# Kernel optimization log

Measured on AMD Instinct MI355X. Metric: run time of the kernel, lower is better.

The kernel has to match this reference:

```python
import jax, jax.numpy as jnp
import numpy as np

G, S, F, H, C, L = 32, 2048, 128, 128, 40, 3
N = G * S           # 65536 nodes
E = N * 16          # 1048576 edges


def setup_inputs() -> dict:
    key = jax.random.key(0)
    ks = jax.random.split(key, 10)
    x = jax.random.normal(ks[0], (N, F), dtype=jnp.float32)
    edge_index = jax.random.randint(ks[1], (2, E), 0, N, dtype=jnp.int64)
    E_meta = jax.random.normal(ks[2], (G, H), dtype=jnp.float32)
    ptr = (jnp.arange(G + 1, dtype=jnp.int64) * S)  # uniform partitions
    # learned params (xavier-ish scaling)
    w0 = jax.random.normal(ks[3], (F, 1), dtype=jnp.float32) * (2.0 / (F + 1)) ** 0.5
    b0 = jax.random.normal(ks[4], (F, H), dtype=jnp.float32) * (2.0 / (F + H)) ** 0.5
    conv_w = jax.random.normal(ks[5], (L, H, H), dtype=jnp.float32) * (1.0 / H) ** 0.5
    conv_b = jnp.zeros((L, H), dtype=jnp.float32)
    lt1_w = jax.random.normal(ks[6], (C, H), dtype=jnp.float32) * (1.0 / H) ** 0.5
    lt1_b = jnp.zeros((C,), dtype=jnp.float32)
    return {"x": x, "edge_index": edge_index, "E_meta": E_meta, "ptr": ptr,
            "w0": w0, "b0": b0, "conv_w": conv_w, "conv_b": conv_b,
            "lt1_w": lt1_w, "lt1_b": lt1_b}


def _gcn_conv(h, src, dst, deg_inv_sqrt, W, b):
    # GCNConv (PyG defaults): h' = D^-1/2 (A+I) D^-1/2 (h W) + b
    hw = h @ W                                          # [N,H]
    norm = deg_inv_sqrt[src] * deg_inv_sqrt[dst]        # [E+N]
    msg = hw[src] * norm[:, None]                       # gather + scale
    return jax.ops.segment_sum(msg, dst, num_segments=h.shape[0]) + b


def reference(x, edge_index, E_meta, ptr, w0, b0, conv_w, conv_b, lt1_w, lt1_b):
    n_nodes = x.shape[0]
    g = E_meta.shape[0]
    s = n_nodes // g  # uniform ptr (ptr[i] = i*s) by construction
    # per-partition dynamic weight: relu(w0 @ emb^T + b0) -> [G,F,H]
    Wdyn = jax.nn.relu(w0[None, :, :] * E_meta[:, None, :] + b0[None, :, :])
    # segment matmul x[ptr[i]:ptr[i+1]] @ Wdyn[i], concatenated -> [N,H]
    h = jnp.einsum('gsf,gfh->gsh', x.reshape(g, s, -1), Wdyn).reshape(n_nodes, -1)
    # add self loops once; symmetric normalization on target degree
    loop = jnp.arange(n_nodes, dtype=edge_index.dtype)
    src = jnp.concatenate([edge_index[0], loop])
    dst = jnp.concatenate([edge_index[1], loop])
    deg = jax.ops.segment_sum(jnp.ones_like(dst, dtype=h.dtype), dst,
                              num_segments=n_nodes)
    deg_inv_sqrt = jnp.where(deg > 0, jax.lax.rsqrt(deg), 0.0)
    for l in range(conv_w.shape[0]):
        h = jax.nn.relu(_gcn_conv(h, src, dst, deg_inv_sqrt, conv_w[l], conv_b[l]))
        # F.dropout with training=False is identity (eval mode)
    logits = h @ lt1_w.T + lt1_b
    return jax.nn.log_softmax(logits, axis=1)
```

## Files before the change

### kernel.cpp

```cpp
#include <hip/hip_runtime.h>

#define NNODES 65536
#define NEDGES 1048576
#define HDIM 128
#define NCLS 40
#define BCAP 6144

#define FP8_SCALE 32.0f
#define FP8_INV   0.03125f

typedef unsigned int uint;
typedef __attribute__((ext_vector_type(8))) short bf16x8;
typedef __attribute__((ext_vector_type(4))) float f32x4;
typedef __attribute__((ext_vector_type(2))) float f32x2;

__device__ __forceinline__ float bf_lo(uint v) {
    return __builtin_bit_cast(float, v << 16);
}
__device__ __forceinline__ float bf_hi(uint v) {
    return __builtin_bit_cast(float, v & 0xffff0000u);
}
__device__ __forceinline__ uint pack_bf16x2(float a, float b) {
    uint ua = __builtin_bit_cast(uint, a);
    uint ub = __builtin_bit_cast(uint, b);
    ua += 0x7fff + ((ua >> 16) & 1);
    ub += 0x7fff + ((ub >> 16) & 1);
    return (ua >> 16) | (ub & 0xffff0000u);
}
__device__ __forceinline__ float tobf(float v) {
    uint u = __builtin_bit_cast(uint, v);
    u += 0x7fff + ((u >> 16) & 1);
    return __builtin_bit_cast(float, u & 0xffff0000u);
}

__device__ __forceinline__ f32x2 fp8_pair(uint u) {
    return __builtin_amdgcn_cvt_pk_f32_fp8((int)u, false);
}

__global__ __launch_bounds__(256) void convT_kernel(
    const float* __restrict__ cw, uint* __restrict__ WT, int* __restrict__ gcursor,
    const float* __restrict__ ltw, uint* __restrict__ WcT8)
{
    int t = threadIdx.x;
    if (blockIdx.x == 0) gcursor[t] = 0;
    int idx = blockIdx.x * 256 + t;
    if (idx < 24576) {
        int ip = idx & 63;
        int o = (idx >> 6) & 127;
        int l = idx >> 13;
        int i0 = ip * 2;
        float v0 = cw[l * 16384 + i0 * 128 + o];
        float v1 = cw[l * 16384 + (i0 + 1) * 128 + o];
        WT[idx] = pack_bf16x2(v0, v1);
    } else {
        int idx2 = idx - 24576;
        int part = (idx2 >= 3072) ? 1 : 0;
        int r = idx2 - part * 3072;
        int o = r >> 6;
        int ip = r & 63;
        float v0 = 0.f, v1 = 0.f;
        if (o < NCLS) {
            float w0v = ltw[o * 128 + ip * 2];
            float w1v = ltw[o * 128 + ip * 2 + 1];
            float h0 = tobf(w0v), h1 = tobf(w1v);
            if (part == 0) { v0 = h0; v1 = h1; }
            else { v0 = w0v - h0; v1 = w1v - h1; }
        }
        WcT8[idx2] = pack_bf16x2(v0, v1);
    }
}

__global__ __launch_bounds__(256) void bucket_scatter(
    const int* __restrict__ src, const int* __restrict__ dst,
    int* __restrict__ gcursor, uint* __restrict__ binned)
{
    __shared__ int lcnt[256];
    __shared__ int lbase[256];
    int t = threadIdx.x;
    int base = blockIdx.x * 4096;
    lcnt[t] = 0;
    __syncthreads();
    uint e[16];
#pragma unroll
    for (int k = 0; k < 16; k++) {
        int i = base + k * 256 + t;
        uint s = (uint)src[i];
        uint d = (uint)dst[i];
        e[k] = (d << 16) | s;
        atomicAdd(&lcnt[d >> 8], 1);
    }
    __syncthreads();
    lbase[t] = t * BCAP + atomicAdd(&gcursor[t], lcnt[t]);
    lcnt[t] = 0;
    __syncthreads();
#pragma unroll
    for (int k = 0; k < 16; k++) {
        int b = e[k] >> 24;
        int r = atomicAdd(&lcnt[b], 1);
        binned[lbase[b] + r] = e[k];
    }
}

__global__ __launch_bounds__(256) void prep_kernel(
    const uint* __restrict__ binned, const int* __restrict__ gcursor,
    int* __restrict__ row_beg, int* __restrict__ row_end4,
    float* __restrict__ dis, int* __restrict__ csr,
    const float* __restrict__ w0, const float* __restrict__ em,
    const float* __restrict__ b0, const uint* __restrict__ convwT0,
    uint* __restrict__ WT)
{
    __shared__ int cnt[256];
    __shared__ int tmp[256];
    __shared__ int fb[256];
    const int t = threadIdx.x;

    if (blockIdx.x < 256) {
        int b = blockIdx.x;
        int e0 = b * BCAP, e1 = e0 + gcursor[b];
        cnt[t] = 0;
        __syncthreads();
        for (int i = e0 + t; i < e1; i += 256)
            atomicAdd(&cnt[(binned[i] >> 16) & 255], 1);
        __syncthreads();
        int v = cnt[t];
        int size4 = (v + 3) & ~3;
        tmp[t] = size4;
        __syncthreads();
        for (int off = 1; off < 256; off <<= 1) {
            int u = (t >= off) ? tmp[t - off] : 0;
            __syncthreads();
            tmp[t] += u;
            __syncthreads();
        }
        fb[t] = tmp[t] - size4;
        int node = (b << 8) + t;
        int beg = e0 + fb[t];
        row_beg[node] = beg;
        row_end4[node] = beg + size4;
        dis[node] = rsqrtf((float)(v + 1));
        for (int p = v; p < size4; p++) csr[beg + p] = NNODES;
        cnt[t] = 0;
        __syncthreads();
        for (int i = e0 + t; i < e1; i += 256) {
            uint e = binned[i];
            int d = (e >> 16) & 255;
            int r = atomicAdd(&cnt[d], 1);
            csr[e0 + fb[d] + r] = (int)(e & 0xffffu);
        }
    } else {
        int bb = blockIdx.x - 256;
        const int g = bb >> 3;
        const int c = bb & 7;
        const int wave = t >> 6;
        const int lane = t & 63;
        const int q = lane >> 4;
        const int l16 = lane & 15;
        const float* emg = em + g * 128;

        f32x4 acc[2];
#pragma unroll
        for (int r = 0; r < 2; r++) {
            acc[r][0] = 0.f; acc[r][1] = 0.f; acc[r][2] = 0.f; acc[r][3] = 0.f;
        }
        const int f = c * 16 + l16;
        const float wf = w0[f];

#pragma unroll
        for (int k0 = 0; k0 < 128; k0 += 32) {
            const int kf = k0 + q * 8;
            bf16x8 afrag[2];
#pragma unroll
            for (int r = 0; r < 2; r++) {
                uint4 u = *(const uint4*)(convwT0 +
                    (size_t)(wave * 32 + r * 16 + l16) * 64 + (kf >> 1));
                afrag[r] = __builtin_bit_cast(bf16x8, u);
            }
            float4 e0 = *(const float4*)(emg + kf);
            float4 e1 = *(const float4*)(emg + kf + 4);
            const float* bp = b0 + (size_t)f * 128 + kf;
            float4 bb0 = *(const float4*)bp;
            float4 bb1 = *(const float4*)(bp + 4);
            float v0 = fmaxf(fmaf(wf, e0.x, bb0.x), 0.f);
            float v1 = fmaxf(fmaf(wf, e0.y, bb0.y), 0.f);
            float v2 = fmaxf(fmaf(wf, e0.z, bb0.z), 0.f);
            float v3 = fmaxf(fmaf(wf, e0.w, bb0.w), 0.f);
            float v4 = fmaxf(fmaf(wf, e1.x, bb1.x), 0.f);
            float v5 = fmaxf(fmaf(wf, e1.y, bb1.y), 0.f);
            float v6 = fmaxf(fmaf(wf, e1.z, bb1.z), 0.f);
            float v7 = fmaxf(fmaf(wf, e1.w, bb1.w), 0.f);
            uint4 u;
            u.x = pack_bf16x2(v0, v1);
            u.y = pack_bf16x2(v2, v3);
            u.z = pack_bf16x2(v4, v5);
            u.w = pack_bf16x2(v6, v7);
            bf16x8 bfrag = __builtin_bit_cast(bf16x8, u);
#pragma unroll
            for (int r = 0; r < 2; r++)
                acc[r] = __builtin_amdgcn_mfma_f32_16x16x32_bf16(
                    afrag[r], bfrag, acc[r], 0, 0, 0);
        }

        uint* WTg = WT + (size_t)g * 8192;
#pragma unroll
        for (int r = 0; r < 2; r++) {
            int o0 = wave * 32 + r * 16 + q * 4;
#pragma unroll
            for (int i = 0; i < 4; i++) {
                int o = o0 + i;
                float v = acc[r][i];
                float w = __shfl_xor(v, 1);
                uint p = (lane & 1) ? pack_bf16x2(w, v) : pack_bf16x2(v, w);
                if (!(lane & 1))
                    WTg[(size_t)o * 64 + (uint)(f >> 1)] = p;
            }
        }
    }
}

__device__ __forceinline__ void store_fp8_row(
    uint* __restrict__ Cp8, int row, float s32, const f32x4* accRC,
    int lane, int l16, int i)
{
#pragma unroll
    for (int c = 0; c < 8; c++) {
        float v = accRC[c][i] * s32;
        float w = __shfl_xor(v, 1);
        int us = __builtin_amdgcn_cvt_pk_fp8_f32(v, w, 0, false);
        uint partner = (uint)__shfl_xor(us, 2);
        if ((lane & 3) == 0) {
            uint p = ((uint)us & 0xffffu) | (partner << 16);
            Cp8[(size_t)row * 32 + c * 4 + (l16 >> 2)] = p;
        }
    }
}

__global__ __launch_bounds__(256) void gemm_mfma(
    const float* __restrict__ A, const uint* __restrict__ BT,
    uint* __restrict__ Cp8, const float* __restrict__ dis, int perGroup)
{
    const int t = threadIdx.x;
    const int wave = t >> 6;
    const int lane = t & 63;
    const int q = lane >> 4;
    const int l16 = lane & 15;
    const int rowBase = blockIdx.x * 128;
    const uint* Bp = perGroup ? BT + ((size_t)(rowBase >> 11) << 13) : BT;

    if (blockIdx.x == 0 && t < 32)
        Cp8[(size_t)NNODES * 32 + t] = 0u;

    f32x4 acc[2][8];
#pragma unroll
    for (int r = 0; r < 2; r++)
#pragma unroll
        for (int c = 0; c < 8; c++) {
            acc[r][c][0] = 0.f; acc[r][c][1] = 0.f;
            acc[r][c][2] = 0.f; acc[r][c][3] = 0.f;
        }

    const int mBase = rowBase + wave * 32 + l16;

#pragma unroll
    for (int k0 = 0; k0 < 128; k0 += 32) {
        const int kf = k0 + q * 8;
        bf16x8 afrag[2];
#pragma unroll
        for (int r = 0; r < 2; r++) {
            const float* ap = A + (size_t)(mBase + r * 16) * 128 + kf;
            float4 a0 = *(const float4*)ap;
            float4 a1 = *(const float4*)(ap + 4);
            uint4 u;
            u.x = pack_bf16x2(a0.x, a0.y);
            u.y = pack_bf16x2(a0.z, a0.w);
            u.z = pack_bf16x2(a1.x, a1.y);
            u.w = pack_bf16x2(a1.z, a1.w);
            afrag[r] = __builtin_bit_cast(bf16x8, u);
        }
#pragma unroll
        for (int c = 0; c < 8; c++) {
            uint4 u = *(const uint4*)(Bp + (size_t)(c * 16 + l16) * 64 + (kf >> 1));
            bf16x8 bfrag = __builtin_bit_cast(bf16x8, u);
#pragma unroll
            for (int r = 0; r < 2; r++)
                acc[r][c] = __builtin_amdgcn_mfma_f32_16x16x32_bf16(
                    afrag[r], bfrag, acc[r][c], 0, 0, 0);
        }
    }

#pragma unroll
    for (int r = 0; r < 2; r++) {
        int row0 = rowBase + wave * 32 + r * 16 + q * 4;
#pragma unroll
        for (int i = 0; i < 4; i++) {
            int row = row0 + i;
            float s32 = dis[row] * FP8_SCALE;
            store_fp8_row(Cp8, row, s32, acc[r], lane, l16, i);
        }
    }
}

__device__ __forceinline__ void aggregate_eighth(
    const uint* __restrict__ hws8_in, const int* __restrict__ row_beg,
    const int* __restrict__ row_end4, const int* __restrict__ csr,
    const float* __restrict__ dis, const float* __restrict__ bias,
    uint* __restrict__ hT, int rowBase, int wave, int lane)
{
    const int g = lane >> 3;
    const int s = lane & 7;
    const int nl = wave * 8 + g;
    const int n = rowBase + nl;
    const int beg = row_beg[n];
    const int end4 = row_end4[n];
    int mx = (end4 - beg) >> 2;
    mx = max(mx, __shfl_xor(mx, 8));
    mx = max(mx, __shfl_xor(mx, 16));
    mx = max(mx, __shfl_xor(mx, 32));

    uint4 su = *((const uint4*)(hws8_in + (size_t)n * 32) + s);
    f32x2 a[8];
    a[0] = fp8_pair(su.x); a[1] = fp8_pair(su.x >> 16);
    a[2] = fp8_pair(su.y); a[3] = fp8_pair(su.y >> 16);
    a[4] = fp8_pair(su.z); a[5] = fp8_pair(su.z >> 16);
    a[6] = fp8_pair(su.w); a[7] = fp8_pair(su.w >> 16);

#define ACC8(u) do { \
        a[0] += fp8_pair((u).x); a[1] += fp8_pair((u).x >> 16); \
        a[2] += fp8_pair((u).y); a[3] += fp8_pair((u).y >> 16); \
        a[4] += fp8_pair((u).z); a[5] += fp8_pair((u).z >> 16); \
        a[6] += fp8_pair((u).w); a[7] += fp8_pair((u).w >> 16); } while (0)

    int i = beg;
    for (int it = 0; it < mx; it += 2, i += 8) {
        int4 sA = *(const int4*)(csr + i);
        int4 sB = *(const int4*)(csr + i + 4);
        if (i >= end4) { sA.x = NNODES; sA.y = NNODES; sA.z = NNODES; sA.w = NNODES; }
        if (i + 4 >= end4) { sB.x = NNODES; sB.y = NNODES; sB.z = NNODES; sB.w = NNODES; }
        uint4 u0 = *((const uint4*)(hws8_in + (size_t)sA.x * 32) + s);
        uint4 u1 = *((const uint4*)(hws8_in + (size_t)sA.y * 32) + s);
        uint4 u2 = *((const uint4*)(hws8_in + (size_t)sA.z * 32) + s);
        uint4 u3 = *((const uint4*)(hws8_in + (size_t)sA.w * 32) + s);
        uint4 u4 = *((const uint4*)(hws8_in + (size_t)sB.x * 32) + s);
        uint4 u5 = *((const uint4*)(hws8_in + (size_t)sB.y * 32) + s);
        uint4 u6 = *((const uint4*)(hws8_in + (size_t)sB.z * 32) + s);
        uint4 u7 = *((const uint4*)(hws8_in + (size_t)sB.w * 32) + s);
        ACC8(u0); ACC8(u1); ACC8(u2); ACC8(u3);
        ACC8(u4); ACC8(u5); ACC8(u6); ACC8(u7);
    }
#undef ACC8

    const float d = dis[n] * FP8_INV;
    const float* bp = bias + s * 16;
    float4 b0 = *(const float4*)bp;
    float4 b1 = *(const float4*)(bp + 4);
    float4 b2 = *(const float4*)(bp + 8);
    float4 b3 = *(const float4*)(bp + 12);
    float o0  = fmaxf(fmaf(d, a[0].x, b0.x), 0.f);
    float o1  = fmaxf(fmaf(d, a[0].y, b0.y), 0.f);
    float o2  = fmaxf(fmaf(d, a[1].x, b0.z), 0.f);
    float o3  = fmaxf(fmaf(d, a[1].y, b0.w), 0.f);
    float o4  = fmaxf(fmaf(d, a[2].x, b1.x), 0.f);
    float o5  = fmaxf(fmaf(d, a[2].y, b1.y), 0.f);
    float o6  = fmaxf(fmaf(d, a[3].x, b1.z), 0.f);
    float o7  = fmaxf(fmaf(d, a[3].y, b1.w), 0.f);
    float o8  = fmaxf(fmaf(d, a[4].x, b2.x), 0.f);
    float o9  = fmaxf(fmaf(d, a[4].y, b2.y), 0.f);
    float o10 = fmaxf(fmaf(d, a[5].x, b2.z), 0.f);
    float o11 = fmaxf(fmaf(d, a[5].y, b2.w), 0.f);
    float o12 = fmaxf(fmaf(d, a[6].x, b3.x), 0.f);
    float o13 = fmaxf(fmaf(d, a[6].y, b3.y), 0.f);
    float o14 = fmaxf(fmaf(d, a[7].x, b3.z), 0.f);
    float o15 = fmaxf(fmaf(d, a[7].y, b3.w), 0.f);
    uint4 w0, w1;
    w0.x = pack_bf16x2(o0, o1);
    w0.y = pack_bf16x2(o2, o3);
    w0.z = pack_bf16x2(o4, o5);
    w0.w = pack_bf16x2(o6, o7);
    w1.x = pack_bf16x2(o8, o9);
    w1.y = pack_bf16x2(o10, o11);
    w1.z = pack_bf16x2(o12, o13);
    w1.w = pack_bf16x2(o14, o15);
    *(uint4*)&hT[nl * 68 + s * 8] = w0;
    *(uint4*)&hT[nl * 68 + s * 8 + 4] = w1;
}

__global__ __launch_bounds__(512) void agg_gemm_kernel(
    const uint* __restrict__ hws8_in, const int* __restrict__ row_beg,
    const int* __restrict__ row_end4, const int* __restrict__ csr,
    const float* __restrict__ dis, const float* __restrict__ bias,
    const uint* __restrict__ BT, uint* __restrict__ out8)
{
    __shared__ uint hT[64 * 68];
    const int t = threadIdx.x;
    const int wave = t >> 6;
    const int lane = t & 63;
    const int rowBase = blockIdx.x * 64;

    if (blockIdx.x == 0 && t < 32)
        out8[(size_t)NNODES * 32 + t] = 0u;

    aggregate_eighth(hws8_in, row_beg, row_end4, csr, dis, bias,
                     hT, rowBase, wave, lane);
    __syncthreads();

    const int q = lane >> 4;
    const int l16 = lane & 15;
    const int mw = wave & 1;
    const int nw = wave >> 1;

    f32x4 acc[2][2];
#pragma unroll
    for (int r = 0; r < 2; r++)
#pragma unroll
        for (int c = 0; c < 2; c++) {
            acc[r][c][0] = 0.f; acc[r][c][1] = 0.f;
            acc[r][c][2] = 0.f; acc[r][c][3] = 0.f;
        }

#pragma unroll
    for (int k0 = 0; k0 < 128; k0 += 32) {
        const int kp = (k0 >> 1) + q * 4;
        bf16x8 afrag[2];
#pragma unroll
        for (int r = 0; r < 2; r++) {
            uint4 u = *(const uint4*)&hT[(mw * 32 + r * 16 + l16) * 68 + kp];
            afrag[r] = __builtin_bit_cast(bf16x8, u);
        }
#pragma unroll
        for (int c = 0; c < 2; c++) {
            uint4 u = *(const uint4*)(BT +
                (size_t)(nw * 32 + c * 16 + l16) * 64 + kp);
            bf16x8 bfrag = __builtin_bit_cast(bf16x8, u);
#pragma unroll
            for (int r = 0; r < 2; r++)
                acc[r][c] = __builtin_amdgcn_mfma_f32_16x16x32_bf16(
                    afrag[r], bfrag, acc[r][c], 0, 0, 0);
        }
    }

#pragma unroll
    for (int r = 0; r < 2; r++) {
        int row0 = rowBase + mw * 32 + r * 16 + q * 4;
#pragma unroll
        for (int i = 0; i < 4; i++) {
            int row = row0 + i;
            float s32 = dis[row] * FP8_SCALE;
#pragma unroll
            for (int c = 0; c < 2; c++) {
                float v = acc[r][c][i] * s32;
                float w = __shfl_xor(v, 1);
                int us = __builtin_amdgcn_cvt_pk_fp8_f32(v, w, 0, false);
                uint partner = (uint)__shfl_xor(us, 2);
                if ((lane & 3) == 0) {
                    uint p = ((uint)us & 0xffffu) | (partner << 16);
                    out8[(size_t)row * 32 + (nw * 2 + c) * 4 + (l16 >> 2)] = p;
                }
            }
        }
    }
}

__global__ __launch_bounds__(512) void agg_logits_kernel(
    const uint* __restrict__ hws8_in, const int* __restrict__ row_beg,
    const int* __restrict__ row_end4, const int* __restrict__ csr,
    const float* __restrict__ dis, const float* __restrict__ bias,
    const uint* __restrict__ WcT8, const float* __restrict__ bc,
    float* __restrict__ out)
{
    __shared__ uint hT[64 * 68];
    const int t = threadIdx.x;
    const int wave = t >> 6;
    const int lane = t & 63;
    const int rowBase = blockIdx.x * 64;

    aggregate_eighth(hws8_in, row_beg, row_end4, csr, dis, bias,
                     hT, rowBase, wave, lane);
    __syncthreads();

    if (wave >= 4) return;

    const int q = lane >> 4;
    const int l16 = lane & 15;

    f32x4 acc[3];
#pragma unroll
    for (int c = 0; c < 3; c++) {
        acc[c][0] = 0.f; acc[c][1] = 0.f; acc[c][2] = 0.f; acc[c][3] = 0.f;
    }

#pragma unroll
    for (int k0 = 0; k0 < 128; k0 += 32) {
        const int kp = (k0 >> 1) + q * 4;
        uint4 ua = *(const uint4*)&hT[(wave * 16 + l16) * 68 + kp];
        bf16x8 af = __builtin_bit_cast(bf16x8, ua);
#pragma unroll
        for (int tile = 0; tile < 3; tile++) {
            uint4 uh = *(const uint4*)(WcT8 + (size_t)(tile * 16 + l16) * 64 + kp);
            uint4 ul = *(const uint4*)(WcT8 + (size_t)(48 + tile * 16 + l16) * 64 + kp);
            acc[tile] = __builtin_amdgcn_mfma_f32_16x16x32_bf16(
                af, __builtin_bit_cast(bf16x8, uh), acc[tile], 0, 0, 0);
            acc[tile] = __builtin_amdgcn_mfma_f32_16x16x32_bf16(
                af, __builtin_bit_cast(bf16x8, ul), acc[tile], 0, 0, 0);
        }
    }

    const float bt0 = bc[l16];
    const float bt1 = bc[16 + l16];
    const float bt2 = (l16 < 8) ? bc[32 + l16] : 0.f;

#pragma unroll
    for (int i = 0; i < 4; i++) {
        const int node = rowBase + wave * 16 + q * 4 + i;
        float g0 = acc[0][i] + bt0;
        float g1 = acc[1][i] + bt1;
        float g2 = (l16 < 8) ? (acc[2][i] + bt2) : -1e30f;
        float m = fmaxf(fmaxf(g0, g1), g2);
        for (int off = 1; off < 16; off <<= 1) m = fmaxf(m, __shfl_xor(m, off));
        float sum = expf(g0 - m) + expf(g1 - m) + ((l16 < 8) ? expf(g2 - m) : 0.f);
        for (int off = 1; off < 16; off <<= 1) sum += __shfl_xor(sum, off);
        float lse = m + logf(sum);
        float* on = out + (size_t)node * NCLS;
        on[l16] = g0 - lse;
        on[16 + l16] = g1 - lse;
        if (l16 < 8) on[32 + l16] = g2 - lse;
    }
}

extern "C" void kernel_launch(void* const* d_in, const int* in_sizes, int n_in,
                              void* d_out, int out_size, void* d_ws, size_t ws_size,
                              hipStream_t stream)
{
    const float* x     = (const float*)d_in[0];
    const int*   ei    = (const int*)d_in[1];
    const float* em    = (const float*)d_in[2];
    const float* w0    = (const float*)d_in[4];
    const float* b0    = (const float*)d_in[5];
    const float* convw = (const float*)d_in[6];
    const float* convb = (const float*)d_in[7];
    const float* ltw   = (const float*)d_in[8];
    const float* ltb   = (const float*)d_in[9];
    float* out = (float*)d_out;

    char* ws = (char*)d_ws;
    size_t off = 0;
    auto alloc = [&](size_t bytes) -> void* {
        void* p = ws + off;
        off += (bytes + 255) & ~(size_t)255;
        return p;
    };
    uint*  hws8A    = (uint*)alloc((size_t)(NNODES + 1) * 32 * 4);
    uint*  hws8B    = (uint*)alloc((size_t)(NNODES + 1) * 32 * 4);
    uint*  WcombT   = (uint*)alloc((size_t)32 * 128 * 64 * 4);
    uint*  convwT   = (uint*)alloc((size_t)3 * 128 * 64 * 4);
    uint*  WcT8     = (uint*)alloc((size_t)96 * 64 * 4);
    int*   gcursor  = (int*)alloc(256 * 4);
    uint*  binned   = (uint*)alloc((size_t)256 * BCAP * 4);
    int*   row_beg  = (int*)alloc((size_t)NNODES * 4);
    int*   row_end4 = (int*)alloc((size_t)NNODES * 4);
    float* dis      = (float*)alloc((size_t)NNODES * 4);
    int*   csr      = (int*)alloc((size_t)256 * BCAP * 4);

    const int* esrc = ei;
    const int* edst = ei + NEDGES;

    convT_kernel<<<120, 256, 0, stream>>>(convw, convwT, gcursor, ltw, WcT8);
    bucket_scatter<<<NEDGES / 4096, 256, 0, stream>>>(esrc, edst, gcursor, binned);
    prep_kernel<<<512, 256, 0, stream>>>(binned, gcursor, row_beg, row_end4, dis,
                                         csr, w0, em, b0, convwT, WcombT);

    gemm_mfma<<<NNODES / 128, 256, 0, stream>>>(x, WcombT, hws8A, dis, 1);

    agg_gemm_kernel<<<NNODES / 64, 512, 0, stream>>>(
        hws8A, row_beg, row_end4, csr, dis, convb + 0 * 128,
        convwT + (size_t)1 * 8192, hws8B);
    agg_gemm_kernel<<<NNODES / 64, 512, 0, stream>>>(
        hws8B, row_beg, row_end4, csr, dis, convb + 1 * 128,
        convwT + (size_t)2 * 8192, hws8A);
    agg_logits_kernel<<<NNODES / 64, 512, 0, stream>>>(
        hws8A, row_beg, row_end4, csr, dis, convb + 2 * 128, WcT8, ltb, out);
}
```

Baseline: 240.6 us.

## Split each CSR row into four source-range quarters for phased neighbour gathers

The CSR build now sub-bins each destination's edges by the top two bits of the source index, giving four padded segments per node with stored end offsets. The aggregation loop walks these quarters in order, so all lanes in a wave gather from roughly the same quarter of the feature table at the same time, which should improve cache locality on the random gathers. The cost is more padding to multiples of 4 per quarter (extra dummy loads), a 4x larger end-offset array, and per-lane divergent loop trip counts instead of the previous wave-uniform max with masking.

```diff
diff --git a/kernel.cpp b/kernel.cpp
--- a/kernel.cpp
+++ b/kernel.cpp
@@ -103,28 +103,33 @@
 
 __global__ __launch_bounds__(256) void prep_kernel(
     const uint* __restrict__ binned, const int* __restrict__ gcursor,
-    int* __restrict__ row_beg, int* __restrict__ row_end4,
+    int* __restrict__ row_beg, int* __restrict__ row_qend,
     float* __restrict__ dis, int* __restrict__ csr,
     const float* __restrict__ w0, const float* __restrict__ em,
     const float* __restrict__ b0, const uint* __restrict__ convwT0,
     uint* __restrict__ WT)
 {
-    __shared__ int cnt[256];
+    __shared__ int cnt4[1024];
+    __shared__ int qb4[1024];
     __shared__ int tmp[256];
-    __shared__ int fb[256];
     const int t = threadIdx.x;
 
     if (blockIdx.x < 256) {
         int b = blockIdx.x;
         int e0 = b * BCAP, e1 = e0 + gcursor[b];
-        cnt[t] = 0;
+        for (int k = t; k < 1024; k += 256) cnt4[k] = 0;
         __syncthreads();
-        for (int i = e0 + t; i < e1; i += 256)
-            atomicAdd(&cnt[(binned[i] >> 16) & 255], 1);
+        for (int i = e0 + t; i < e1; i += 256) {
+            uint e = binned[i];
+            atomicAdd(&cnt4[(((e >> 16) & 255) << 2) + ((e & 0xffffu) >> 14)], 1);
+        }
         __syncthreads();
-        int v = cnt[t];
-        int size4 = (v + 3) & ~3;
-        tmp[t] = size4;
+        int c0 = cnt4[t * 4 + 0], c1 = cnt4[t * 4 + 1];
+        int c2 = cnt4[t * 4 + 2], c3 = cnt4[t * 4 + 3];
+        int s0 = (c0 + 3) & ~3, s1 = (c1 + 3) & ~3;
+        int s2 = (c2 + 3) & ~3, s3 = (c3 + 3) & ~3;
+        int tot = s0 + s1 + s2 + s3;
+        tmp[t] = tot;
         __syncthreads();
         for (int off = 1; off < 256; off <<= 1) {
             int u = (t >= off) ? tmp[t - off] : 0;
@@ -132,20 +137,30 @@
             tmp[t] += u;
             __syncthreads();
         }
-        fb[t] = tmp[t] - size4;
+        int beg = e0 + tmp[t] - tot;
         int node = (b << 8) + t;
-        int beg = e0 + fb[t];
         row_beg[node] = beg;
-        row_end4[node] = beg + size4;
-        dis[node] = rsqrtf((float)(v + 1));
-        for (int p = v; p < size4; p++) csr[beg + p] = NNODES;
-        cnt[t] = 0;
+        int q0e = beg + s0, q1e = q0e + s1, q2e = q1e + s2, q3e = q2e + s3;
+        int4 qe; qe.x = q0e; qe.y = q1e; qe.z = q2e; qe.w = q3e;
+        ((int4*)row_qend)[node] = qe;
+        qb4[t * 4 + 0] = beg;
+        qb4[t * 4 + 1] = q0e;
+        qb4[t * 4 + 2] = q1e;
+        qb4[t * 4 + 3] = q2e;
+        dis[node] = rsqrtf((float)(c0 + c1 + c2 + c3 + 1));
+        for (int p = c0; p < s0; p++) csr[beg + p] = NNODES;
+        for (int p = c1; p < s1; p++) csr[q0e + p] = NNODES;
+        for (int p = c2; p < s2; p++) csr[q1e + p] = NNODES;
+        for (int p = c3; p < s3; p++) csr[q2e + p] = NNODES;
+        __syncthreads();
+        for (int k = t; k < 1024; k += 256) cnt4[k] = 0;
         __syncthreads();
         for (int i = e0 + t; i < e1; i += 256) {
             uint e = binned[i];
-            int d = (e >> 16) & 255;
-            int r = atomicAdd(&cnt[d], 1);
-            csr[e0 + fb[d] + r] = (int)(e & 0xffffu);
+            int s = (int)(e & 0xffffu);
+            int idx4 = (((e >> 16) & 255) << 2) + (s >> 14);
+            int r = atomicAdd(&cnt4[idx4], 1);
+            csr[qb4[idx4] + r] = s;
         }
     } else {
         int bb = blockIdx.x - 256;
@@ -301,7 +316,7 @@
 
 __device__ __forceinline__ void aggregate_eighth(
     const uint* __restrict__ hws8_in, const int* __restrict__ row_beg,
-    const int* __restrict__ row_end4, const int* __restrict__ csr,
+    const int* __restrict__ row_qend, const int* __restrict__ csr,
     const float* __restrict__ dis, const float* __restrict__ bias,
     uint* __restrict__ hT, int rowBase, int wave, int lane)
 {
@@ -309,12 +324,8 @@
     const int s = lane & 7;
     const int nl = wave * 8 + g;
     const int n = rowBase + nl;
-    const int beg = row_beg[n];
-    const int end4 = row_end4[n];
-    int mx = (end4 - beg) >> 2;
-    mx = max(mx, __shfl_xor(mx, 8));
-    mx = max(mx, __shfl_xor(mx, 16));
-    mx = max(mx, __shfl_xor(mx, 32));
+    int st = row_beg[n];
+    const int4 qe = ((const int4*)row_qend)[n];
 
     uint4 su = *((const uint4*)(hws8_in + (size_t)n * 32) + s);
     f32x2 a[8];
@@ -329,22 +340,18 @@
         a[4] += fp8_pair((u).z); a[5] += fp8_pair((u).z >> 16); \
         a[6] += fp8_pair((u).w); a[7] += fp8_pair((u).w >> 16); } while (0)
 
-    int i = beg;
-    for (int it = 0; it < mx; it += 2, i += 8) {
-        int4 sA = *(const int4*)(csr + i);
-        int4 sB = *(const int4*)(csr + i + 4);
-        if (i >= end4) { sA.x = NNODES; sA.y = NNODES; sA.z = NNODES; sA.w = NNODES; }
-        if (i + 4 >= end4) { sB.x = NNODES; sB.y = NNODES; sB.z = NNODES; sB.w = NNODES; }
-        uint4 u0 = *((const uint4*)(hws8_in + (size_t)sA.x * 32) + s);
-        uint4 u1 = *((const uint4*)(hws8_in + (size_t)sA.y * 32) + s);
-        uint4 u2 = *((const uint4*)(hws8_in + (size_t)sA.z * 32) + s);
-        uint4 u3 = *((const uint4*)(hws8_in + (size_t)sA.w * 32) + s);
-        uint4 u4 = *((const uint4*)(hws8_in + (size_t)sB.x * 32) + s);
-        uint4 u5 = *((const uint4*)(hws8_in + (size_t)sB.y * 32) + s);
-        uint4 u6 = *((const uint4*)(hws8_in + (size_t)sB.z * 32) + s);
-        uint4 u7 = *((const uint4*)(hws8_in + (size_t)sB.w * 32) + s);
-        ACC8(u0); ACC8(u1); ACC8(u2); ACC8(u3);
-        ACC8(u4); ACC8(u5); ACC8(u6); ACC8(u7);
+#pragma unroll
+    for (int qq = 0; qq < 4; qq++) {
+        const int en = (qq == 0) ? qe.x : (qq == 1) ? qe.y : (qq == 2) ? qe.z : qe.w;
+        for (int i = st; i < en; i += 4) {
+            int4 sA = *(const int4*)(csr + i);
+            uint4 u0 = *((const uint4*)(hws8_in + (size_t)sA.x * 32) + s);
+            uint4 u1 = *((const uint4*)(hws8_in + (size_t)sA.y * 32) + s);
+            uint4 u2 = *((const uint4*)(hws8_in + (size_t)sA.z * 32) + s);
+            uint4 u3 = *((const uint4*)(hws8_in + (size_t)sA.w * 32) + s);
+            ACC8(u0); ACC8(u1); ACC8(u2); ACC8(u3);
+        }
+        st = en;
     }
 #undef ACC8
 
@@ -385,7 +392,7 @@
 
 __global__ __launch_bounds__(512) void agg_gemm_kernel(
     const uint* __restrict__ hws8_in, const int* __restrict__ row_beg,
-    const int* __restrict__ row_end4, const int* __restrict__ csr,
+    const int* __restrict__ row_qend, const int* __restrict__ csr,
     const float* __restrict__ dis, const float* __restrict__ bias,
     const uint* __restrict__ BT, uint* __restrict__ out8)
 {
@@ -398,7 +405,7 @@
     if (blockIdx.x == 0 && t < 32)
         out8[(size_t)NNODES * 32 + t] = 0u;
 
-    aggregate_eighth(hws8_in, row_beg, row_end4, csr, dis, bias,
+    aggregate_eighth(hws8_in, row_beg, row_qend, csr, dis, bias,
                      hT, rowBase, wave, lane);
     __syncthreads();
 
@@ -461,7 +468,7 @@
 
 __global__ __launch_bounds__(512) void agg_logits_kernel(
     const uint* __restrict__ hws8_in, const int* __restrict__ row_beg,
-    const int* __restrict__ row_end4, const int* __restrict__ csr,
+    const int* __restrict__ row_qend, const int* __restrict__ csr,
     const float* __restrict__ dis, const float* __restrict__ bias,
     const uint* __restrict__ WcT8, const float* __restrict__ bc,
     float* __restrict__ out)
@@ -472,7 +479,7 @@
     const int lane = t & 63;
     const int rowBase = blockIdx.x * 64;
 
-    aggregate_eighth(hws8_in, row_beg, row_end4, csr, dis, bias,
+    aggregate_eighth(hws8_in, row_beg, row_qend, csr, dis, bias,
                      hT, rowBase, wave, lane);
     __syncthreads();
 
@@ -555,7 +562,7 @@
     int*   gcursor  = (int*)alloc(256 * 4);
     uint*  binned   = (uint*)alloc((size_t)256 * BCAP * 4);
     int*   row_beg  = (int*)alloc((size_t)NNODES * 4);
-    int*   row_end4 = (int*)alloc((size_t)NNODES * 4);
+    int*   row_qend = (int*)alloc((size_t)NNODES * 16);
     float* dis      = (float*)alloc((size_t)NNODES * 4);
     int*   csr      = (int*)alloc((size_t)256 * BCAP * 4);
 
@@ -564,17 +571,17 @@
 
     convT_kernel<<<120, 256, 0, stream>>>(convw, convwT, gcursor, ltw, WcT8);
     bucket_scatter<<<NEDGES / 4096, 256, 0, stream>>>(esrc, edst, gcursor, binned);
-    prep_kernel<<<512, 256, 0, stream>>>(binned, gcursor, row_beg, row_end4, dis,
+    prep_kernel<<<512, 256, 0, stream>>>(binned, gcursor, row_beg, row_qend, dis,
                                          csr, w0, em, b0, convwT, WcombT);
 
     gemm_mfma<<<NNODES / 128, 256, 0, stream>>>(x, WcombT, hws8A, dis, 1);
 
     agg_gemm_kernel<<<NNODES / 64, 512, 0, stream>>>(
-        hws8A, row_beg, row_end4, csr, dis, convb + 0 * 128,
+        hws8A, row_beg, row_qend, csr, dis, convb + 0 * 128,
         convwT + (size_t)1 * 8192, hws8B);
     agg_gemm_kernel<<<NNODES / 64, 512, 0, stream>>>(
-        hws8B, row_beg, row_end4, csr, dis, convb + 1 * 128,
+        hws8B, row_beg, row_qend, csr, dis, convb + 1 * 128,
         convwT + (size_t)2 * 8192, hws8A);
     agg_logits_kernel<<<NNODES / 64, 512, 0, stream>>>(
-        hws8A, row_beg, row_end4, csr, dis, convb + 2 * 128, WcT8, ltb, out);
-}
+        hws8A, row_beg, row_qend, csr, dis, convb + 2 * 128, WcT8, ltb, out);
+}
```

Result: no change. 238.3 us (-0.9%).
